# Performance work log

Measured on AMD Instinct MI355X. Metric: run time of the kernel, lower is better.

Reference implementation:

```python
import jax, jax.numpy as jnp
import numpy as np

B, S, HID = 2, 2048, 2048
H, HK, D = 32, 8, 64
N_REP = H // HK
SCALE = D ** -0.5


def setup_inputs() -> dict:
    key = jax.random.key(0)
    ks = jax.random.split(key, 9)
    std = HID ** -0.5
    causal = jnp.tril(jnp.ones((S, S), dtype=bool))
    attention_mask = jnp.where(causal, 0.0, -1e9).astype(jnp.float32)[None, None]  # [1,1,S,S]
    return {
        "hidden_states": jax.random.normal(ks[0], (B, S, HID), jnp.float32),
        "attention_mask": attention_mask,
        "q_w": jax.random.normal(ks[1], (HID, H * D), jnp.float32) * std,
        "q_b": jax.random.normal(ks[2], (H * D,), jnp.float32) * 0.01,
        "k_w": jax.random.normal(ks[3], (HID, HK * D), jnp.float32) * std,
        "k_b": jax.random.normal(ks[4], (HK * D,), jnp.float32) * 0.01,
        "v_w": jax.random.normal(ks[5], (HID, HK * D), jnp.float32) * std,
        "v_b": jax.random.normal(ks[6], (HK * D,), jnp.float32) * 0.01,
        "dense_w": jax.random.normal(ks[7], (HID, HID), jnp.float32) * std,
        "dense_b": jax.random.normal(ks[8], (HID,), jnp.float32) * 0.01,
    }


def reference(hidden_states, attention_mask, q_w, q_b, k_w, k_b, v_w, v_b, dense_w, dense_b):
    b, s, _ = hidden_states.shape
    # projections -> [b, h, s, d]
    q = (hidden_states @ q_w + q_b).reshape(b, s, H, D).transpose(0, 2, 1, 3)
    k = (hidden_states @ k_w + k_b).reshape(b, s, HK, D).transpose(0, 2, 1, 3)
    v = (hidden_states @ v_w + v_b).reshape(b, s, HK, D).transpose(0, 2, 1, 3)
    # GQA: repeat_kv (repeat_interleave along head dim)
    k = jnp.repeat(k, N_REP, axis=1)  # [b, H, s, d]
    v = jnp.repeat(v, N_REP, axis=1)
    # eager attention: full score matrix
    scores = jnp.einsum("bhqd,bhkd->bhqk", q, k) * SCALE + attention_mask
    w = jax.nn.softmax(scores.astype(jnp.float32), axis=-1).astype(q.dtype)
    attn = jnp.einsum("bhqk,bhkd->bhqd", w, v)
    attn = attn.transpose(0, 2, 1, 3).reshape(b, s, H * D)
    return attn @ dense_w + dense_b
```

## Files before the change

### kernel.cpp

```cpp
#include <hip/hip_runtime.h>
#include <hip/hip_bf16.h>


typedef short s16x8 __attribute__((ext_vector_type(8)));
typedef float f32x4 __attribute__((ext_vector_type(4)));

static constexpr int BB = 2, SS = 2048, HID = 2048, HH = 32, HKV = 8, DD = 64;
static constexpr int MM = BB * SS;
static constexpr int NQKV = 3072;

#define DEV __device__ __forceinline__

DEV short f2bf(float f) {
    unsigned u = __builtin_bit_cast(unsigned, f);
    return (short)((u + 0x7fffu + ((u >> 16) & 1u)) >> 16);
}

DEV unsigned cvtpk(float lo, float hi) {
    unsigned r;
    asm("v_cvt_pk_bf16_f32 %0, %1, %2" : "=v"(r) : "v"(lo), "v"(hi));
    return r;
}

DEV void stage16(const short* gsrc, short* lbase) {
    __builtin_amdgcn_global_load_lds((const __attribute__((address_space(1))) void*)gsrc,
                                     (__attribute__((address_space(3))) void*)lbase, 16, 0, 0);
}

__global__ __launch_bounds__(256) void cvt_f32_bf16(const float* __restrict__ in,
                                                    short* __restrict__ out, int n) {
    int i = (blockIdx.x * 256 + threadIdx.x) * 8;
    if (i >= n) return;
    float4 a = *reinterpret_cast<const float4*>(in + i);
    float4 b = *reinterpret_cast<const float4*>(in + i + 4);
    s16x8 o;
    o[0] = f2bf(a.x); o[1] = f2bf(a.y); o[2] = f2bf(a.z); o[3] = f2bf(a.w);
    o[4] = f2bf(b.x); o[5] = f2bf(b.y); o[6] = f2bf(b.z); o[7] = f2bf(b.w);
    *reinterpret_cast<s16x8*>(out + i) = o;
}

__global__ __launch_bounds__(256) void transpose_cvt(const float* __restrict__ in,
                                                     short* __restrict__ out,
                                                     int K, int N) {
    __shared__ float tile[32][33];
    int k0 = blockIdx.x * 32, n0 = blockIdx.y * 32;
    int tx = threadIdx.x & 31, ty = threadIdx.x >> 5;
#pragma unroll
    for (int r = ty; r < 32; r += 8)
        tile[r][tx] = in[(size_t)(k0 + r) * N + n0 + tx];
    __syncthreads();
#pragma unroll
    for (int r = ty; r < 32; r += 8)
        out[(size_t)(n0 + r) * K + k0 + tx] = f2bf(tile[tx][r]);
}

__global__ __launch_bounds__(256) void transpose_v(const short* __restrict__ QKV,
                                                   short* __restrict__ Vtg) {
    __shared__ int tile[32][33];
    const int s0 = blockIdx.x * 32, c0 = blockIdx.y * 32, b = blockIdx.z;
    const int tx = threadIdx.x & 31, ty = threadIdx.x >> 5;
#pragma unroll
    for (int r = ty; r < 32; r += 8)
        tile[r][tx] = QKV[(size_t)(b * SS + s0 + r) * NQKV + 2560 + c0 + tx];
    __syncthreads();
#pragma unroll
    for (int r = ty; r < 32; r += 8) {
        const int c = c0 + r;
        Vtg[((size_t)(b * HKV + (c >> 6)) * 64 + (c & 63)) * SS + s0 + tx] = (short)tile[tx][r];
    }
}

__global__ __launch_bounds__(256) void concat_bias(const float* __restrict__ qb,
                                                   const float* __restrict__ kb,
                                                   const float* __restrict__ vb,
                                                   float* __restrict__ cb) {
    int i = blockIdx.x * 256 + threadIdx.x;
    if (i < 2048) cb[i] = qb[i];
    else if (i < 2560) cb[i] = kb[i - 2048];
    else if (i < 3072) cb[i] = vb[i - 2560];
}

template <int BM, int BN, typename OutT>
__global__ __launch_bounds__(512) void gemm8p(const short* __restrict__ A,
                                              const short* __restrict__ Bt,
                                              const float* __restrict__ bias,
                                              OutT* __restrict__ C,
                                              int M, int N, int K, int qcols) {
    constexpr int NR = BN / 64;
    constexpr int ACH = BM * 4;
    constexpr int BCH = BN * 4;
    static_assert(ACH % 512 == 0, "A chunks per half must be thread-uniform");
    constexpr int SA = ACH / 512;
    __shared__ __align__(16) short lds[(BM + BN) * 128];
    const int tid = threadIdx.x, lane = tid & 63, wid = tid >> 6;
    const int fr = lane & 15, fk = lane >> 4;
    const int wm = wid >> 2, wn = wid & 3;
    const int nbn = N / BN;
    const int cpx = gridDim.x >> 3;
    const int wg = (blockIdx.x & 7) * cpx + (blockIdx.x >> 3);
    const int bm = wg / nbn, bn = wg % nbn;
    const int NT = K / 64;

    const short* Ablk = A + (size_t)bm * BM * K;
    const short* Bblk = Bt + (size_t)bn * BN * K;

    auto abase = [&](int bf, int kh) { return bf * (BM * 64) + kh * (BM * 32); };
    auto bbase = [&](int bf, int kh) { return 2 * (BM * 64) + bf * (BN * 64) + kh * (BN * 32); };

    auto stA = [&](int bf, int kh, int kt) {
#pragma unroll
        for (int l = 0; l < SA; ++l) {
            const int c = l * 512 + tid;
            const int r = c >> 2, sg = (c & 3) ^ ((r >> 1) & 3);
            stage16(Ablk + (size_t)r * K + kt + kh * 32 + sg * 8,
                    &lds[abase(bf, kh) + (l * 512 + wid * 64) * 8]);
        }
    };
    auto stB = [&](int bf, int kh, int kt) {
        {
            const int c = tid;
            const int r = c >> 2, sg = (c & 3) ^ ((r >> 1) & 3);
            stage16(Bblk + (size_t)r * K + kt + kh * 32 + sg * 8,
                    &lds[bbase(bf, kh) + (wid * 64) * 8]);
        }
        if constexpr (BCH > 512) {
            if (tid < BCH - 512) {
                const int c = 512 + tid;
                const int r = c >> 2, sg = (c & 3) ^ ((r >> 1) & 3);
                stage16(Bblk + (size_t)r * K + kt + kh * 32 + sg * 8,
                        &lds[bbase(bf, kh) + ((512 + wid * 64)) * 8]);
            }
        }
    };

    auto waithalf = [&](bool pf) {
        if (!pf) { asm volatile("s_waitcnt vmcnt(0)" ::: "memory"); return; }
        if constexpr (BCH > 512) {
            if (wid < (BCH - 512) / 64) asm volatile("s_waitcnt vmcnt(4)" ::: "memory");
            else                        asm volatile("s_waitcnt vmcnt(3)" ::: "memory");
        } else {
            asm volatile("s_waitcnt vmcnt(3)" ::: "memory");
        }
    };

    f32x4 acc[8][NR] = {};

    stA(0, 0, 0); stB(0, 0, 0);
    stA(0, 1, 0); stB(0, 1, 0);
    waithalf(true);
    asm volatile("s_barrier" ::: "memory");

    for (int t = 0; t < NT; ++t) {
        const int bf = t & 1, sf = bf ^ 1;
        const int ktn = (t + 1) * 64;
        const bool pf = (t + 1 < NT);
#pragma unroll
        for (int kh = 0; kh < 2; ++kh) {
            s16x8 bfrag[NR], afrag[8];
#pragma unroll
            for (int n = 0; n < NR; ++n) {
                const int row = wn * (BN / 4) + n * 16 + fr;
                bfrag[n] = *reinterpret_cast<const s16x8*>(
                    &lds[bbase(bf, kh) + row * 32 + ((fk ^ ((row >> 1) & 3)) * 8)]);
            }
#pragma unroll
            for (int i = 0; i < 8; ++i) {
                const int row = wm * 128 + i * 16 + fr;
                afrag[i] = *reinterpret_cast<const s16x8*>(
                    &lds[abase(bf, kh) + row * 32 + ((fk ^ ((row >> 1) & 3)) * 8)]);
            }
            if (pf) stA(sf, kh, ktn);
            __builtin_amdgcn_s_setprio(1);
#pragma unroll
            for (int i = 0; i < 4; ++i)
#pragma unroll
                for (int n = 0; n < NR; ++n)
                    acc[i][n] = __builtin_amdgcn_mfma_f32_16x16x32_bf16(
                        afrag[i], bfrag[n], acc[i][n], 0, 0, 0);
            __builtin_amdgcn_s_setprio(0);
            if (pf) stB(sf, kh, ktn);
            __builtin_amdgcn_s_setprio(1);
#pragma unroll
            for (int i = 4; i < 8; ++i)
#pragma unroll
                for (int n = 0; n < NR; ++n)
                    acc[i][n] = __builtin_amdgcn_mfma_f32_16x16x32_bf16(
                        afrag[i], bfrag[n], acc[i][n], 0, 0, 0);
            __builtin_amdgcn_s_setprio(0);
            waithalf(pf);
            asm volatile("s_barrier" ::: "memory");
        }
    }

#pragma unroll
    for (int n = 0; n < NR; ++n) {
        const int col = bn * BN + wn * (BN / 4) + n * 16 + fr;
        const float bv = bias[col];
        const float sc = (col < qcols) ? 0.125f : 1.0f;
#pragma unroll
        for (int mi = 0; mi < 8; ++mi) {
            const int row0 = bm * BM + wm * 128 + mi * 16 + fk * 4;
#pragma unroll
            for (int r = 0; r < 4; ++r) {
                const float v = (acc[mi][n][r] + bv) * sc;
                if constexpr (sizeof(OutT) == 2)
                    reinterpret_cast<short*>(C)[(size_t)(row0 + r) * N + col] = f2bf(v);
                else
                    reinterpret_cast<float*>(C)[(size_t)(row0 + r) * N + col] = v;
            }
        }
    }
}

__global__ __launch_bounds__(256, 2) void attn_fwd(
        const short* __restrict__ QKV,
        const short* __restrict__ Vtg,
        short* __restrict__ Ob) {
    constexpr int KB = 64;
    __shared__ __align__(16) short Qs[128 * 64];
    __shared__ __align__(16) short Ks[2][KB * 64];
    __shared__ __align__(16) short Vt[2][64 * 64];
    __shared__ __align__(16) short Ps[128 * 64];

    const int pair = blockIdx.x;
    const int bh = blockIdx.y;
    const int b = bh >> 5, h = bh & 31;
    const int kvh = h >> 2;
    const int tid = threadIdx.x, lane = tid & 63, wid = tid >> 6;
    const int fr = lane & 15, fk = lane >> 4;
    const int wq0 = wid * 32;

    const short* kbase = QKV + (size_t)b * SS * NQKV + 2048 + kvh * DD;
    const short* vbase = Vtg + (size_t)(b * HKV + kvh) * 64 * SS;

    auto stageKV = [&](int bb, int kv0) {
#pragma unroll
        for (int is = 0; is < 2; ++is) {
            const int c = is * 256 + wid * 64 + lane;
            const int r = c >> 3, sg = (c & 7) ^ (r & 7);
            stage16(kbase + (size_t)(kv0 + r) * NQKV + sg * 8,
                    &Ks[bb][(is * 256 + wid * 64) * 8]);
            stage16(vbase + (size_t)r * SS + kv0 + sg * 8,
                    &Vt[bb][(is * 256 + wid * 64) * 8]);
        }
    };
    auto stageQ = [&](int q0) {
        const short* qbase = QKV + ((size_t)b * SS + q0) * NQKV + h * DD;
#pragma unroll
        for (int is = 0; is < 4; ++is) {
            const int c = is * 256 + wid * 64 + lane;
            const int r = c >> 3, sg = (c & 7) ^ (r & 7);
            stage16(qbase + (size_t)r * NQKV + sg * 8,
                    &Qs[(is * 256 + wid * 64) * 8]);
        }
    };

    s16x8 ones = {};
    if (fr == 0) {
#pragma unroll
        for (int e = 0; e < 8; ++e) ones[e] = (short)0x3F80;
    }

    int cur = 0;
    stageQ(pair * 128);
    stageKV(0, 0);

    for (int sidx = 0; sidx < 2; ++sidx) {
        const int strip = sidx ? (15 - pair) : pair;
        const int q0 = strip * 128;
        const size_t qrow0 = (size_t)b * SS + q0;
        const int nt = 2 * strip + 2;

        __syncthreads();

        s16x8 bq[2][2];
#pragma unroll
        for (int i = 0; i < 2; ++i)
#pragma unroll
            for (int ks = 0; ks < 2; ++ks) {
                const int row = wq0 + i * 16 + fr;
                const int byte = (ks * 64 + fk * 16) ^ ((row & 7) << 4);
                bq[i][ks] = *reinterpret_cast<const s16x8*>(
                    reinterpret_cast<const char*>(Qs) + row * 128 + byte);
            }

        f32x4 acc_o[2][4] = {};
        f32x4 acc_l[2] = {};

        for (int t = 0; t < nt; ++t) {
            const int kv0 = t * KB;
            if (t + 1 < nt) {
                stageKV(cur ^ 1, kv0 + KB);
            } else if (sidx == 0) {
                stageQ((15 - pair) * 128);
                stageKV(cur ^ 1, 0);
            }

            f32x4 sacc[2][4] = {};
            __builtin_amdgcn_s_setprio(1);
#pragma unroll
            for (int j = 0; j < 4; ++j)
#pragma unroll
                for (int ks = 0; ks < 2; ++ks) {
                    const int row = j * 16 + fr;
                    const int byte = (ks * 64 + fk * 16) ^ ((row & 7) << 4);
                    s16x8 kf = *reinterpret_cast<const s16x8*>(
                        reinterpret_cast<const char*>(Ks[cur]) + row * 128 + byte);
#pragma unroll
                    for (int i = 0; i < 2; ++i)
                        sacc[i][j] = __builtin_amdgcn_mfma_f32_16x16x32_bf16(kf, bq[i][ks], sacc[i][j], 0, 0, 0);
                }
            __builtin_amdgcn_s_setprio(0);

            if (kv0 + KB - 1 > q0 + wq0) {
#pragma unroll
                for (int i = 0; i < 2; ++i) {
                    const int qg = q0 + wq0 + i * 16 + fr;
#pragma unroll
                    for (int j = 0; j < 4; ++j) {
                        const int kvb = kv0 + j * 16 + fk * 4;
#pragma unroll
                        for (int r = 0; r < 4; ++r)
                            if (kvb + r > qg) sacc[i][j][r] = -INFINITY;
                    }
                }
            }

#pragma unroll
            for (int i = 0; i < 2; ++i) {
                char* pbase = reinterpret_cast<char*>(Ps) + (wq0 + i * 16 + fr) * 128;
#pragma unroll
                for (int j = 0; j < 4; ++j)
#pragma unroll
                    for (int hh = 0; hh < 2; ++hh) {
                        const unsigned pw = cvtpk(__expf(sacc[i][j][2 * hh]),
                                                  __expf(sacc[i][j][2 * hh + 1]));
                        const int byte = ((j * 8 + fk * 2 + hh) << 2) ^ ((fr & 7) << 4);
                        *reinterpret_cast<unsigned*>(pbase + byte) = pw;
                    }
            }

            s16x8 ap[2][2];
#pragma unroll
            for (int i = 0; i < 2; ++i) {
                const char* pbase = reinterpret_cast<const char*>(Ps) + (wq0 + i * 16 + fr) * 128;
#pragma unroll
                for (int ks = 0; ks < 2; ++ks) {
                    const int byte = ((ks * 4 + fk) * 16) ^ ((fr & 7) << 4);
                    ap[i][ks] = *reinterpret_cast<const s16x8*>(pbase + byte);
                }
            }

            __builtin_amdgcn_s_setprio(1);
#pragma unroll
            for (int jd = 0; jd < 4; ++jd)
#pragma unroll
                for (int ks = 0; ks < 2; ++ks) {
                    const int row = jd * 16 + fr;
                    const int byte = (ks * 64 + fk * 16) ^ ((row & 7) << 4);
                    s16x8 bv = *reinterpret_cast<const s16x8*>(
                        reinterpret_cast<const char*>(Vt[cur]) + row * 128 + byte);
#pragma unroll
                    for (int i = 0; i < 2; ++i)
                        acc_o[i][jd] = __builtin_amdgcn_mfma_f32_16x16x32_bf16(ap[i][ks], bv, acc_o[i][jd], 0, 0, 0);
                }
#pragma unroll
            for (int i = 0; i < 2; ++i)
#pragma unroll
                for (int ks = 0; ks < 2; ++ks)
                    acc_l[i] = __builtin_amdgcn_mfma_f32_16x16x32_bf16(ap[i][ks], ones, acc_l[i], 0, 0, 0);
            __builtin_amdgcn_s_setprio(0);

            __syncthreads();
            cur ^= 1;
        }

#pragma unroll
        for (int i = 0; i < 2; ++i)
#pragma unroll
            for (int r = 0; r < 4; ++r) {
                const float l = __shfl(acc_l[i][r], (lane & 48));
                const float inv = 1.f / l;
                const size_t grow = (qrow0 + wq0 + i * 16 + fk * 4 + r) * (size_t)(HH * DD) + h * DD;
#pragma unroll
                for (int jd = 0; jd < 4; ++jd)
                    Ob[grow + jd * 16 + fr] = f2bf(acc_o[i][jd][r] * inv);
            }
    }
}

extern "C" void kernel_launch(void* const* d_in, const int* in_sizes, int n_in,
                              void* d_out, int out_size, void* d_ws, size_t ws_size,
                              hipStream_t stream) {
    const float* hidden  = (const float*)d_in[0];
    const float* q_w     = (const float*)d_in[2];
    const float* q_b     = (const float*)d_in[3];
    const float* k_w     = (const float*)d_in[4];
    const float* k_b     = (const float*)d_in[5];
    const float* v_w     = (const float*)d_in[6];
    const float* v_b     = (const float*)d_in[7];
    const float* dense_w = (const float*)d_in[8];
    const float* dense_b = (const float*)d_in[9];
    float* out = (float*)d_out;

    short* wt   = (short*)d_ws;
    short* dwt  = wt + 6291456;
    short* QKV  = dwt + 4194304;
    short* Vtg  = QKV + 12582912;
    short* hidb = Vtg + 2097152;
    short* Ob   = hidb;
    float* cbias = (float*)(hidb + 8388608);

    cvt_f32_bf16<<<4096, 256, 0, stream>>>(hidden, hidb, MM * HID);
    transpose_cvt<<<dim3(64, 64), 256, 0, stream>>>(q_w, wt, HID, HH * DD);
    transpose_cvt<<<dim3(64, 16), 256, 0, stream>>>(k_w, wt + 2048 * 2048, HID, HKV * DD);
    transpose_cvt<<<dim3(64, 16), 256, 0, stream>>>(v_w, wt + 2560 * 2048, HID, HKV * DD);
    transpose_cvt<<<dim3(64, 64), 256, 0, stream>>>(dense_w, dwt, HID, HID);
    concat_bias<<<12, 256, 0, stream>>>(q_b, k_b, v_b, cbias);

    gemm8p<256, 192, short><<<256, 512, 0, stream>>>(hidb, wt, cbias, QKV, MM, NQKV, HID, 2048);

    transpose_v<<<dim3(64, 16, 2), 256, 0, stream>>>(QKV, Vtg);

    attn_fwd<<<dim3(8, 64), 256, 0, stream>>>(QKV, Vtg, Ob);

    gemm8p<256, 128, float><<<256, 512, 0, stream>>>(Ob, dwt, dense_b, out, MM, HID, HID, 0);
}
```

Baseline: 181.0 us.

## Add 128x128 GEMM for output projection and merge weight transpose launches

Replaces the 256x128-tile, 512-thread output projection GEMM with a new 128x128-tile, 256-thread kernel. It uses double-buffered global-to-LDS staging, swizzled LDS reads and MFMA issue interleaved with prefetch, and launches 512 workgroups instead of 256. The aim is better CU occupancy and load balance on the dense projection, at the cost of less data reuse per tile. Separately, the four weight transpose-convert launches are merged into two by using a z grid dimension, which cuts launch overhead.

```diff
diff --git a/kernel.cpp b/kernel.cpp
--- a/kernel.cpp
+++ b/kernel.cpp
@@ -39,10 +39,14 @@
     *reinterpret_cast<s16x8*>(out + i) = o;
 }
 
-__global__ __launch_bounds__(256) void transpose_cvt(const float* __restrict__ in,
-                                                     short* __restrict__ out,
-                                                     int K, int N) {
+__global__ __launch_bounds__(256) void transpose_cvt2(const float* __restrict__ in0,
+                                                      short* __restrict__ out0,
+                                                      const float* __restrict__ in1,
+                                                      short* __restrict__ out1,
+                                                      int K, int N) {
     __shared__ float tile[32][33];
+    const float* in = blockIdx.z ? in1 : in0;
+    short* out = blockIdx.z ? out1 : out0;
     int k0 = blockIdx.x * 32, n0 = blockIdx.y * 32;
     int tx = threadIdx.x & 31, ty = threadIdx.x >> 5;
 #pragma unroll
@@ -212,6 +216,113 @@
     }
 }
 
+__global__ __launch_bounds__(256) void gemm128(const short* __restrict__ A,
+                                               const short* __restrict__ Bt,
+                                               const float* __restrict__ bias,
+                                               float* __restrict__ C,
+                                               int M, int N, int K) {
+    __shared__ __align__(16) short lds[256 * 128];
+    const int tid = threadIdx.x, lane = tid & 63, wid = tid >> 6;
+    const int fr = lane & 15, fk = lane >> 4;
+    const int wm = wid >> 1, wn = wid & 1;
+    const int nbn = N / 128;
+    const int cpx = gridDim.x >> 3;
+    const int wg = (blockIdx.x & 7) * cpx + (blockIdx.x >> 3);
+    const int bm = wg / nbn, bn = wg % nbn;
+    const int NT = K / 64;
+
+    const short* Ablk = A + (size_t)bm * 128 * K;
+    const short* Bblk = Bt + (size_t)bn * 128 * K;
+
+    auto abase = [&](int bf, int kh) { return bf * (128 * 64) + kh * (128 * 32); };
+    auto bbase = [&](int bf, int kh) { return 2 * (128 * 64) + bf * (128 * 64) + kh * (128 * 32); };
+
+    auto stA = [&](int bf, int kh, int kt) {
+#pragma unroll
+        for (int l = 0; l < 2; ++l) {
+            const int c = l * 256 + tid;
+            const int r = c >> 2, sg = (c & 3) ^ ((r >> 1) & 3);
+            stage16(Ablk + (size_t)r * K + kt + kh * 32 + sg * 8,
+                    &lds[abase(bf, kh) + (l * 256 + wid * 64) * 8]);
+        }
+    };
+    auto stB = [&](int bf, int kh, int kt) {
+#pragma unroll
+        for (int l = 0; l < 2; ++l) {
+            const int c = l * 256 + tid;
+            const int r = c >> 2, sg = (c & 3) ^ ((r >> 1) & 3);
+            stage16(Bblk + (size_t)r * K + kt + kh * 32 + sg * 8,
+                    &lds[bbase(bf, kh) + (l * 256 + wid * 64) * 8]);
+        }
+    };
+    auto waithalf = [&](bool pf) {
+        if (pf) asm volatile("s_waitcnt vmcnt(4)" ::: "memory");
+        else    asm volatile("s_waitcnt vmcnt(0)" ::: "memory");
+    };
+
+    f32x4 acc[4][4] = {};
+
+    stA(0, 0, 0); stB(0, 0, 0);
+    stA(0, 1, 0); stB(0, 1, 0);
+    waithalf(true);
+    asm volatile("s_barrier" ::: "memory");
+
+    for (int t = 0; t < NT; ++t) {
+        const int bf = t & 1, sf = bf ^ 1;
+        const int ktn = (t + 1) * 64;
+        const bool pf = (t + 1 < NT);
+#pragma unroll
+        for (int kh = 0; kh < 2; ++kh) {
+            s16x8 bfrag[4], afrag[4];
+#pragma unroll
+            for (int n = 0; n < 4; ++n) {
+                const int row = wn * 64 + n * 16 + fr;
+                bfrag[n] = *reinterpret_cast<const s16x8*>(
+                    &lds[bbase(bf, kh) + row * 32 + ((fk ^ ((row >> 1) & 3)) * 8)]);
+            }
+#pragma unroll
+            for (int i = 0; i < 4; ++i) {
+                const int row = wm * 64 + i * 16 + fr;
+                afrag[i] = *reinterpret_cast<const s16x8*>(
+                    &lds[abase(bf, kh) + row * 32 + ((fk ^ ((row >> 1) & 3)) * 8)]);
+            }
+            if (pf) stA(sf, kh, ktn);
+            __builtin_amdgcn_s_setprio(1);
+#pragma unroll
+            for (int i = 0; i < 2; ++i)
+#pragma unroll
+                for (int n = 0; n < 4; ++n)
+                    acc[i][n] = __builtin_amdgcn_mfma_f32_16x16x32_bf16(
+                        afrag[i], bfrag[n], acc[i][n], 0, 0, 0);
+            __builtin_amdgcn_s_setprio(0);
+            if (pf) stB(sf, kh, ktn);
+            __builtin_amdgcn_s_setprio(1);
+#pragma unroll
+            for (int i = 2; i < 4; ++i)
+#pragma unroll
+                for (int n = 0; n < 4; ++n)
+                    acc[i][n] = __builtin_amdgcn_mfma_f32_16x16x32_bf16(
+                        afrag[i], bfrag[n], acc[i][n], 0, 0, 0);
+            __builtin_amdgcn_s_setprio(0);
+            waithalf(pf);
+            asm volatile("s_barrier" ::: "memory");
+        }
+    }
+
+#pragma unroll
+    for (int n = 0; n < 4; ++n) {
+        const int col = bn * 128 + wn * 64 + n * 16 + fr;
+        const float bv = bias[col];
+#pragma unroll
+        for (int mi = 0; mi < 4; ++mi) {
+            const int row0 = bm * 128 + wm * 64 + mi * 16 + fk * 4;
+#pragma unroll
+            for (int r = 0; r < 4; ++r)
+                C[(size_t)(row0 + r) * N + col] = acc[mi][n][r] + bv;
+        }
+    }
+}
+
 __global__ __launch_bounds__(256, 2) void attn_fwd(
         const short* __restrict__ QKV,
         const short* __restrict__ Vtg,
@@ -412,10 +523,9 @@
     float* cbias = (float*)(hidb + 8388608);
 
     cvt_f32_bf16<<<4096, 256, 0, stream>>>(hidden, hidb, MM * HID);
-    transpose_cvt<<<dim3(64, 64), 256, 0, stream>>>(q_w, wt, HID, HH * DD);
-    transpose_cvt<<<dim3(64, 16), 256, 0, stream>>>(k_w, wt + 2048 * 2048, HID, HKV * DD);
-    transpose_cvt<<<dim3(64, 16), 256, 0, stream>>>(v_w, wt + 2560 * 2048, HID, HKV * DD);
-    transpose_cvt<<<dim3(64, 64), 256, 0, stream>>>(dense_w, dwt, HID, HID);
+    transpose_cvt2<<<dim3(64, 64, 2), 256, 0, stream>>>(q_w, wt, dense_w, dwt, HID, HID);
+    transpose_cvt2<<<dim3(64, 16, 2), 256, 0, stream>>>(k_w, wt + 2048 * 2048,
+                                                        v_w, wt + 2560 * 2048, HID, HKV * DD);
     concat_bias<<<12, 256, 0, stream>>>(q_b, k_b, v_b, cbias);
 
     gemm8p<256, 192, short><<<256, 512, 0, stream>>>(hidb, wt, cbias, QKV, MM, NQKV, HID, 2048);
@@ -424,5 +534,5 @@
 
     attn_fwd<<<dim3(8, 64), 256, 0, stream>>>(QKV, Vtg, Ob);
 
-    gemm8p<256, 128, float><<<256, 512, 0, stream>>>(Ob, dwt, dense_b, out, MM, HID, HID, 0);
-}
+    gemm128<<<512, 256, 0, stream>>>(Ob, dwt, dense_b, out, MM, HID, HID);
+}
```

Measured after the change: 177.3 us. -2.0%, faster.
